# Kernel optimization log

Measured on AMD Instinct MI355X. Metric: run time of the kernel, lower is better.

The kernel has to match this reference:

```python
import jax, jax.numpy as jnp
import numpy as np

N_CHILDS = 50000
N_EDGES = 500000
NODE_FEAT = 256
NUM_SEM = 57
HID = 256
EDGE_FEAT = 64
EDGE_TYPES = 4
NUM_ITERS = 2


def setup_inputs() -> dict:
    key = jax.random.key(0)
    ks = jax.random.split(key, 12)
    d_in = NODE_FEAT + NUM_SEM            # 313
    d_ne = 2 * HID + EDGE_FEAT + EDGE_TYPES  # 580
    d_par = HID * (NUM_ITERS + 1)         # 768
    def lin(k, fan_in, fan_out):
        kw, kb = jax.random.split(k)
        s = 1.0 / np.sqrt(fan_in)
        return (jax.random.uniform(kw, (fan_in, fan_out), jnp.float32, -s, s),
                jax.random.uniform(kb, (fan_out,), jnp.float32, -s, s))
    W_child, b_child = lin(ks[0], d_in, HID)
    W_ne0, b_ne0 = lin(ks[1], d_ne, HID)
    W_ne1, b_ne1 = lin(ks[2], d_ne, HID)
    W_parent, b_parent = lin(ks[3], d_par, NODE_FEAT)
    return {
        "child_feats": jax.random.normal(ks[4], (1, N_CHILDS, d_in), jnp.float32),
        "child_exists": jnp.ones((1, N_CHILDS, 1), jnp.float32),
        "edge_type_onehot": jax.random.normal(ks[5], (1, N_EDGES, EDGE_TYPES), jnp.float32),
        "edge_feats": jax.random.normal(ks[6], (1, N_EDGES, EDGE_FEAT), jnp.float32),
        "edge_indices": jax.random.randint(ks[7], (1, N_EDGES, 2), 0, N_CHILDS, jnp.int64),
        "W_child": W_child, "b_child": b_child,
        "W_ne0": W_ne0, "b_ne0": b_ne0,
        "W_ne1": W_ne1, "b_ne1": b_ne1,
        "W_parent": W_parent, "b_parent": b_parent,
    }


def reference(child_feats, child_exists, edge_type_onehot, edge_feats, edge_indices,
              W_child, b_child, W_ne0, b_ne0, W_ne1, b_ne1, W_parent, b_parent):
    n = child_feats.shape[1]
    # node embedding: linear + relu, mask non-existent children
    x = jax.nn.relu(jnp.einsum('bnd,dh->bnh', child_feats, W_child) + b_child)
    x = x * child_exists                              # [1, N, H]
    iter_parent = [x.max(axis=1)]                     # symmetric_type == 'max'
    ef = jnp.concatenate([edge_type_onehot, edge_feats], axis=2)[0]  # [E, 4+64]
    src = edge_indices[0, :, 0]
    dst = edge_indices[0, :, 1]
    cnt = jax.ops.segment_sum(jnp.ones((src.shape[0],), x.dtype), src, num_segments=n)
    denom = jnp.maximum(cnt, 1.0)[:, None]            # scatter_mean clamp
    for W, b in ((W_ne0, b_ne0), (W_ne1, b_ne1)):
        nef = jnp.concatenate([x[0, src], x[0, dst], ef], axis=1)  # [E, 580]
        nef = jax.nn.relu(nef @ W + b)                # [E, H]
        # edge_symmetric_type == 'avg': scatter_mean over source index
        x = (jax.ops.segment_sum(nef, src, num_segments=n) / denom)[None]
        iter_parent.append(x.max(axis=1))
    parent = jnp.concatenate(iter_parent, axis=1)     # [1, H*(iters+1)]
    return jax.nn.relu(parent @ W_parent + b_parent)  # [1, node_feat_size]
```

## Files before the change

kernel.cpp:

```cpp
#include <hip/hip_runtime.h>

#define NC   50000
#define NE   500000
#define NEP  (NE + 64)
#define DIN  313
#define DNE  580
#define KPC  320
#define KB   96
#define NB_SCAN 196

typedef __attribute__((ext_vector_type(8))) short bf16x8;
typedef __attribute__((ext_vector_type(4))) float f32x4;

static __device__ __forceinline__ unsigned short f2bf(float f) {
    unsigned u = __float_as_uint(f);
    unsigned r = (u + 0x7fff + ((u >> 16) & 1)) >> 16;
    return (unsigned short)r;
}
static __device__ __forceinline__ float bf2f(unsigned short u) {
    return __uint_as_float(((unsigned)u) << 16);
}
static __device__ __forceinline__ void gload_lds16(const unsigned short* g, unsigned short* l) {
    __builtin_amdgcn_global_load_lds(
        (const __attribute__((address_space(1))) unsigned int*)(g),
        (__attribute__((address_space(3))) unsigned int*)(l), 16, 0, 0);
}

__global__ __launch_bounds__(256) void prep_w_kernel(
    const float* __restrict__ W0, const float* __restrict__ W1,
    const float* __restrict__ Wc,
    unsigned short* __restrict__ Wpt, unsigned short* __restrict__ Wbt,
    unsigned short* __restrict__ Wct)
{
    int b = blockIdx.x;
    if (b < 1024) {
        int layer = b >> 9, n2 = b & 511;
        const float* W = layer ? W1 : W0;
        unsigned short* dst = Wpt + (size_t)layer * 512 * 256 + (size_t)n2 * 256;
        int t = threadIdx.x;
        int ch = t >> 5, s = (t >> 3) & 3, j = t & 7;
        int gk = ch * 32 + ((s ^ (n2 & 3)) * 8) + j;
        float v = (n2 < 256) ? W[(size_t)gk * 256 + n2] : W[(size_t)(256 + gk) * 256 + (n2 - 256)];
        dst[t] = f2bf(v);
    } else if (b < 1536) {
        int idx = b - 1024;
        int layer = idx >> 8, n = idx & 255;
        const float* W = layer ? W1 : W0;
        unsigned short* dst = Wbt + (size_t)layer * 256 * KB + (size_t)n * KB;
        int t = threadIdx.x;
        if (t < KB) {
            int ch = t >> 5, s = (t >> 3) & 3, j = t & 7;
            int gk = ch * 32 + ((s ^ (n & 3)) * 8) + j;
            float v = (512 + gk < DNE) ? W[(size_t)(512 + gk) * 256 + n] : 0.0f;
            dst[t] = f2bf(v);
        }
    } else {
        int n = b - 1536;
        unsigned short* dst = Wct + (size_t)n * KPC;
        for (int t = threadIdx.x; t < KPC; t += 256) {
            int ch = t >> 5, s = (t >> 3) & 3, j = t & 7;
            int gk = ch * 32 + ((s ^ (n & 3)) * 8) + j;
            float v = (gk < DIN) ? Wc[(size_t)gk * 256 + n] : 0.0f;
            dst[t] = f2bf(v);
        }
    }
}

__global__ __launch_bounds__(256, 4) void child_mfma_kernel(
    const float* __restrict__ cf, const float* __restrict__ exists,
    const unsigned short* __restrict__ Wct, const float* __restrict__ bias,
    unsigned short* __restrict__ xb, float* __restrict__ pmax)
{
    __shared__ unsigned short sA[64][40];
    __shared__ unsigned short sB[256][32];
    __shared__ float smax[256];

    const int tid = threadIdx.x, lane = tid & 63, wid = tid >> 6;
    const int wm = wid >> 1, wn = wid & 1, l15 = lane & 15, l4 = lane >> 4;
    const int node0 = blockIdx.x * 64;
    const int arow = tid >> 2, s3 = tid & 3;

    smax[tid] = 0.0f;

    f32x4 acc[2][8];
    #pragma unroll
    for (int mi = 0; mi < 2; ++mi)
        #pragma unroll
        for (int ni = 0; ni < 8; ++ni)
            acc[mi][ni] = (f32x4){0.f, 0.f, 0.f, 0.f};

    int nodeA = node0 + arow; if (nodeA >= NC) nodeA = NC - 1;

    for (int ch = 0; ch < 10; ++ch) {
        #pragma unroll
        for (int i = 0; i < 4; ++i) {
            int n = (wid << 6) + (i << 4) + (lane >> 2);
            gload_lds16(Wct + (size_t)n * KPC + ch * 32 + (lane & 3) * 8,
                        &sB[(wid << 6) + (i << 4)][0]);
        }
        {
            int gk0 = ch * 32 + s3 * 8;
            union { unsigned short u[8]; int4 v; } pk;
            #pragma unroll
            for (int j = 0; j < 8; ++j) {
                int gk = gk0 + j;
                float f = (gk < DIN) ? cf[(size_t)nodeA * DIN + gk] : 0.0f;
                pk.u[j] = f2bf(f);
            }
            *(int4*)&sA[arow][s3 * 8] = pk.v;
        }
        __syncthreads();
        bf16x8 af[2];
        #pragma unroll
        for (int mi = 0; mi < 2; ++mi)
            af[mi] = *(const bf16x8*)&sA[wm * 32 + mi * 16 + l15][l4 * 8];
        #pragma unroll
        for (int ni = 0; ni < 8; ++ni) {
            int n = wn * 128 + ni * 16 + l15;
            bf16x8 bfr = *(const bf16x8*)&sB[n][(l4 ^ (n & 3)) * 8];
            acc[0][ni] = __builtin_amdgcn_mfma_f32_16x16x32_bf16(af[0], bfr, acc[0][ni], 0, 0, 0);
            acc[1][ni] = __builtin_amdgcn_mfma_f32_16x16x32_bf16(af[1], bfr, acc[1][ni], 0, 0, 0);
        }
        __syncthreads();
    }

    float bv[8];
    #pragma unroll
    for (int ni = 0; ni < 8; ++ni) bv[ni] = bias[wn * 128 + ni * 16 + l15];
    float cmax[8];
    #pragma unroll
    for (int ni = 0; ni < 8; ++ni) cmax[ni] = 0.0f;

    #pragma unroll
    for (int mi = 0; mi < 2; ++mi) {
        #pragma unroll
        for (int r = 0; r < 4; ++r) {
            int node = node0 + wm * 32 + mi * 16 + l4 * 4 + r;
            if (node < NC) {
                float ex = exists[node];
                #pragma unroll
                for (int ni = 0; ni < 8; ++ni) {
                    float v = fmaxf(acc[mi][ni][r] + bv[ni], 0.f) * ex;
                    xb[(size_t)node * 256 + wn * 128 + ni * 16 + l15] = f2bf(v);
                    cmax[ni] = fmaxf(cmax[ni], v);
                }
            }
        }
    }
    #pragma unroll
    for (int ni = 0; ni < 8; ++ni)
        atomicMax((unsigned int*)&smax[wn * 128 + ni * 16 + l15], __float_as_uint(cmax[ni]));
    __syncthreads();
    atomicMax((unsigned int*)&pmax[tid], __float_as_uint(smax[tid]));
}

__global__ __launch_bounds__(256, 3) void node_gemm_kernel(
    const unsigned short* __restrict__ xb,
    const unsigned short* __restrict__ Wpt,
    unsigned short* __restrict__ yp)
{
    __shared__ unsigned short sA[2][64][40];
    __shared__ unsigned short sB[2][256][32];

    const int tid = threadIdx.x, lane = tid & 63, wid = tid >> 6;
    const int wm = wid >> 1, wn = wid & 1, l15 = lane & 15, l4 = lane >> 4;
    const int node0 = blockIdx.x * 64;
    const int n0 = blockIdx.y * 256;
    const int arow = tid >> 2, s3 = tid & 3;

    int nodeA = node0 + arow; if (nodeA >= NC) nodeA = NC - 1;

    f32x4 acc[2][8];
    #pragma unroll
    for (int mi = 0; mi < 2; ++mi)
        #pragma unroll
        for (int ni = 0; ni < 8; ++ni)
            acc[mi][ni] = (f32x4){0.f, 0.f, 0.f, 0.f};

    #pragma unroll
    for (int i = 0; i < 4; ++i) {
        int n = (wid << 6) + (i << 4) + (lane >> 2);
        gload_lds16(Wpt + (size_t)(n0 + n) * 256 + (lane & 3) * 8, &sB[0][(wid << 6) + (i << 4)][0]);
    }
    *(int4*)&sA[0][arow][s3 * 8] = *(const int4*)(xb + (size_t)nodeA * 256 + s3 * 8);
    __syncthreads();

    int buf = 0;
    for (int ch = 0; ch < 8; ++ch) {
        const int nch = ch + 1;
        int4 areg;
        if (nch < 8) {
            #pragma unroll
            for (int i = 0; i < 4; ++i) {
                int n = (wid << 6) + (i << 4) + (lane >> 2);
                gload_lds16(Wpt + (size_t)(n0 + n) * 256 + nch * 32 + (lane & 3) * 8,
                            &sB[buf ^ 1][(wid << 6) + (i << 4)][0]);
            }
            areg = *(const int4*)(xb + (size_t)nodeA * 256 + nch * 32 + s3 * 8);
        }
        bf16x8 af[2];
        #pragma unroll
        for (int mi = 0; mi < 2; ++mi)
            af[mi] = *(const bf16x8*)&sA[buf][wm * 32 + mi * 16 + l15][l4 * 8];
        #pragma unroll
        for (int ni = 0; ni < 8; ++ni) {
            int n = wn * 128 + ni * 16 + l15;
            bf16x8 bfr = *(const bf16x8*)&sB[buf][n][(l4 ^ (n & 3)) * 8];
            acc[0][ni] = __builtin_amdgcn_mfma_f32_16x16x32_bf16(af[0], bfr, acc[0][ni], 0, 0, 0);
            acc[1][ni] = __builtin_amdgcn_mfma_f32_16x16x32_bf16(af[1], bfr, acc[1][ni], 0, 0, 0);
        }
        if (nch < 8) *(int4*)&sA[buf ^ 1][arow][s3 * 8] = areg;
        __syncthreads();
        buf ^= 1;
    }

    #pragma unroll
    for (int mi = 0; mi < 2; ++mi) {
        #pragma unroll
        for (int r = 0; r < 4; ++r) {
            int node = node0 + wm * 32 + mi * 16 + l4 * 4 + r;
            if (node < NC) {
                #pragma unroll
                for (int ni = 0; ni < 8; ++ni)
                    yp[(size_t)node * 512 + n0 + wn * 128 + ni * 16 + l15] = f2bf(acc[mi][ni][r]);
            }
        }
    }
}

__global__ __launch_bounds__(256, 3) void node_gemm_scaled_kernel(
    const float* __restrict__ accb, const float* __restrict__ invv,
    const unsigned short* __restrict__ Wpt,
    unsigned short* __restrict__ yp)
{
    __shared__ unsigned short sA[2][64][40];
    __shared__ unsigned short sB[2][256][32];

    const int tid = threadIdx.x, lane = tid & 63, wid = tid >> 6;
    const int wm = wid >> 1, wn = wid & 1, l15 = lane & 15, l4 = lane >> 4;
    const int node0 = blockIdx.x * 64;
    const int n0 = blockIdx.y * 256;
    const int arow = tid >> 2, s3 = tid & 3;

    int nodeA = node0 + arow; if (nodeA >= NC) nodeA = NC - 1;
    const float inv_n = invv[nodeA];

    f32x4 acc[2][8];
    #pragma unroll
    for (int mi = 0; mi < 2; ++mi)
        #pragma unroll
        for (int ni = 0; ni < 8; ++ni)
            acc[mi][ni] = (f32x4){0.f, 0.f, 0.f, 0.f};

    #pragma unroll
    for (int i = 0; i < 4; ++i) {
        int n = (wid << 6) + (i << 4) + (lane >> 2);
        gload_lds16(Wpt + (size_t)(n0 + n) * 256 + (lane & 3) * 8, &sB[0][(wid << 6) + (i << 4)][0]);
    }
    {
        float4 a0 = *(const float4*)(accb + (size_t)nodeA * 256 + s3 * 8);
        float4 a1 = *(const float4*)(accb + (size_t)nodeA * 256 + s3 * 8 + 4);
        union { unsigned short u[8]; int4 v; } pk;
        pk.u[0]=f2bf(a0.x*inv_n); pk.u[1]=f2bf(a0.y*inv_n); pk.u[2]=f2bf(a0.z*inv_n); pk.u[3]=f2bf(a0.w*inv_n);
        pk.u[4]=f2bf(a1.x*inv_n); pk.u[5]=f2bf(a1.y*inv_n); pk.u[6]=f2bf(a1.z*inv_n); pk.u[7]=f2bf(a1.w*inv_n);
        *(int4*)&sA[0][arow][s3 * 8] = pk.v;
    }
    __syncthreads();

    int buf = 0;
    for (int ch = 0; ch < 8; ++ch) {
        const int nch = ch + 1;
        float4 f4a, f4b;
        if (nch < 8) {
            #pragma unroll
            for (int i = 0; i < 4; ++i) {
                int n = (wid << 6) + (i << 4) + (lane >> 2);
                gload_lds16(Wpt + (size_t)(n0 + n) * 256 + nch * 32 + (lane & 3) * 8,
                            &sB[buf ^ 1][(wid << 6) + (i << 4)][0]);
            }
            f4a = *(const float4*)(accb + (size_t)nodeA * 256 + nch * 32 + s3 * 8);
            f4b = *(const float4*)(accb + (size_t)nodeA * 256 + nch * 32 + s3 * 8 + 4);
        }
        bf16x8 af[2];
        #pragma unroll
        for (int mi = 0; mi < 2; ++mi)
            af[mi] = *(const bf16x8*)&sA[buf][wm * 32 + mi * 16 + l15][l4 * 8];
        #pragma unroll
        for (int ni = 0; ni < 8; ++ni) {
            int n = wn * 128 + ni * 16 + l15;
            bf16x8 bfr = *(const bf16x8*)&sB[buf][n][(l4 ^ (n & 3)) * 8];
            acc[0][ni] = __builtin_amdgcn_mfma_f32_16x16x32_bf16(af[0], bfr, acc[0][ni], 0, 0, 0);
            acc[1][ni] = __builtin_amdgcn_mfma_f32_16x16x32_bf16(af[1], bfr, acc[1][ni], 0, 0, 0);
        }
        if (nch < 8) {
            union { unsigned short u[8]; int4 v; } pk;
            pk.u[0]=f2bf(f4a.x*inv_n); pk.u[1]=f2bf(f4a.y*inv_n); pk.u[2]=f2bf(f4a.z*inv_n); pk.u[3]=f2bf(f4a.w*inv_n);
            pk.u[4]=f2bf(f4b.x*inv_n); pk.u[5]=f2bf(f4b.y*inv_n); pk.u[6]=f2bf(f4b.z*inv_n); pk.u[7]=f2bf(f4b.w*inv_n);
            *(int4*)&sA[buf ^ 1][arow][s3 * 8] = pk.v;
        }
        __syncthreads();
        buf ^= 1;
    }

    #pragma unroll
    for (int mi = 0; mi < 2; ++mi) {
        #pragma unroll
        for (int r = 0; r < 4; ++r) {
            int node = node0 + wm * 32 + mi * 16 + l4 * 4 + r;
            if (node < NC) {
                #pragma unroll
                for (int ni = 0; ni < 8; ++ni)
                    yp[(size_t)node * 512 + n0 + wn * 128 + ni * 16 + l15] = f2bf(acc[mi][ni][r]);
            }
        }
    }
}

__global__ __launch_bounds__(256) void count_int_kernel(
    const int* __restrict__ eidx, int* __restrict__ icnt)
{
    int t = blockIdx.x * 256 + threadIdx.x;
    if (t < NE) atomicAdd(&icnt[eidx[2 * t]], 1);
}

__global__ __launch_bounds__(256) void scan1_kernel(
    const int* __restrict__ icnt, int* __restrict__ part)
{
    __shared__ int sd[256];
    int i = blockIdx.x * 256 + threadIdx.x;
    sd[threadIdx.x] = (i < NC) ? icnt[i] : 0;
    __syncthreads();
    for (int d = 128; d > 0; d >>= 1) {
        if (threadIdx.x < d) sd[threadIdx.x] += sd[threadIdx.x + d];
        __syncthreads();
    }
    if (threadIdx.x == 0) part[blockIdx.x] = sd[0];
}

__global__ void scan2_kernel(int* __restrict__ part)
{
    if (threadIdx.x == 0) {
        int acc = 0;
        for (int i = 0; i < NB_SCAN; ++i) { int v = part[i]; part[i] = acc; acc += v; }
    }
}

__global__ __launch_bounds__(256) void scan3_kernel(
    const int* __restrict__ icnt, const int* __restrict__ part,
    int* __restrict__ cur)
{
    __shared__ int sc[256];
    const int t = threadIdx.x;
    int i = blockIdx.x * 256 + t;
    int val = (i < NC) ? icnt[i] : 0;
    sc[t] = val;
    __syncthreads();
    for (int d = 1; d < 256; d <<= 1) {
        int x = (t >= d) ? sc[t - d] : 0;
        __syncthreads();
        sc[t] += x;
        __syncthreads();
    }
    if (i < NC) cur[i] = part[blockIdx.x] + sc[t] - val;
}

__global__ __launch_bounds__(256) void bin_kernel(
    const int* __restrict__ eidx, int* __restrict__ cur, int* __restrict__ perm)
{
    int t = blockIdx.x * 256 + threadIdx.x;
    if (t < NE) {
        int s = eidx[2 * t];
        int p = atomicAdd(&cur[s], 1);
        perm[p] = t;
    }
}

__global__ __launch_bounds__(256) void inv_kernel(
    const int* __restrict__ icnt, float* __restrict__ inv)
{
    int t = blockIdx.x * 256 + threadIdx.x;
    if (t < NC) inv[t] = 1.0f / fmaxf((float)icnt[t], 1.0f);
}

__global__ __launch_bounds__(256) void ef_prep_kernel(
    const float* __restrict__ eto, const float* __restrict__ efe,
    const int* __restrict__ perm, const int* __restrict__ eidx,
    unsigned short* __restrict__ efc01, unsigned short* __restrict__ efc2,
    int* __restrict__ esrc, int* __restrict__ edst)
{
    int p = blockIdx.x * 256 + threadIdx.x;
    if (p >= NE) return;
    int e = perm[p];
    esrc[p] = eidx[2 * e];
    edst[p] = eidx[2 * e + 1];
    const float* efr = efe + (size_t)e * 64;

    union { unsigned short u[8]; int4 v; } pk;
    {
        float4 a = *(const float4*)(eto + (size_t)e * 4);
        float4 b = *(const float4*)(efr + 0);
        pk.u[0]=f2bf(a.x); pk.u[1]=f2bf(a.y); pk.u[2]=f2bf(a.z); pk.u[3]=f2bf(a.w);
        pk.u[4]=f2bf(b.x); pk.u[5]=f2bf(b.y); pk.u[6]=f2bf(b.z); pk.u[7]=f2bf(b.w);
        *(int4*)(efc01 + (size_t)p * 32) = pk.v;
    }
    #pragma unroll
    for (int g = 1; g < 4; ++g) {
        float4 a = *(const float4*)(efr + g * 8 - 4);
        float4 b = *(const float4*)(efr + g * 8);
        pk.u[0]=f2bf(a.x); pk.u[1]=f2bf(a.y); pk.u[2]=f2bf(a.z); pk.u[3]=f2bf(a.w);
        pk.u[4]=f2bf(b.x); pk.u[5]=f2bf(b.y); pk.u[6]=f2bf(b.z); pk.u[7]=f2bf(b.w);
        *(int4*)(efc01 + (size_t)p * 32 + g * 8) = pk.v;
    }
    #pragma unroll
    for (int g = 0; g < 4; ++g) {
        float4 a = *(const float4*)(efr + 28 + g * 8);
        float4 b = *(const float4*)(efr + 32 + g * 8);
        pk.u[0]=f2bf(a.x); pk.u[1]=f2bf(a.y); pk.u[2]=f2bf(a.z); pk.u[3]=f2bf(a.w);
        pk.u[4]=f2bf(b.x); pk.u[5]=f2bf(b.y); pk.u[6]=f2bf(b.z); pk.u[7]=f2bf(b.w);
        *(int4*)(efc01 + ((size_t)NEP + p) * 32 + g * 8) = pk.v;
    }
    {
        float4 a = *(const float4*)(efr + 60);
        pk.u[0]=f2bf(a.x); pk.u[1]=f2bf(a.y); pk.u[2]=f2bf(a.z); pk.u[3]=f2bf(a.w);
        pk.u[4]=0; pk.u[5]=0; pk.u[6]=0; pk.u[7]=0;
        *(int4*)(efc2 + (size_t)p * 8) = pk.v;
    }
}

#define LOAD16(B, YT, YM)                                              \
    _Pragma("unroll")                                                  \
    for (int r = 0; r < 16; ++r) {                                     \
        int row = (B) * 16 + r;                                        \
        int sr_ = s_src[row];                                          \
        if (sr_ != ldsrc) {                   \
            ytPrev = bf2f(yp[((unsigned)sr_ << 9) + (unsigned)col]);   \
            ldsrc = sr_;                                               \
        }                                                              \
        YT[r] = ytPrev;                                                \
        YM[r] = bf2f(yp[((unsigned)s_dst[row] << 9) + 256u + (unsigned)col]); \
    }

#define WALK16(B, YT, YM)                                              \
    _Pragma("unroll")                                                  \
    for (int r = 0; r < 16; ++r) {                                     \
        int row = (B) * 16 + r;                                        \
        float v = 0.0f;                                                \
        if (e0 + row < NE)                                             \
            v = fmaxf(bf2f(epb[row][col]) + YT[r] + YM[r] + b_col, 0.f); \
        int sr = s_src[row];                                           \
        if (sr != curn) {                                              \
            if (rstart > 0) accb[(size_t)curn * 256 + col] = run;      \
            else            atomicAdd(&accb[(size_t)curn * 256 + col], run); \
            curn = sr; run = v; rstart = row;                          \
        } else {                                                       \
            run += v;                                                  \
        }                                                              \
    }

__global__ __launch_bounds__(256, 4) void combine_efc_kernel(
    const unsigned short* __restrict__ yp,
    const unsigned short* __restrict__ efc01,
    const unsigned short* __restrict__ efc2,
    const int* __restrict__ esrc, const int* __restrict__ edst,
    const unsigned short* __restrict__ Wbt,
    const float* __restrict__ bias,
    float* __restrict__ accb)
{
    __shared__ __align__(16) unsigned char smem[34816];
    unsigned short (*sA01)[64][32] = (unsigned short (*)[64][32])(smem);
    unsigned short (*sA2)[8]       = (unsigned short (*)[8])(smem + 8192);
    unsigned short (*sW)[32]       = (unsigned short (*)[32])(smem + 9216);
    unsigned short (*epb)[272]     = (unsigned short (*)[272])(smem);
    __shared__ int s_src[64], s_dst[64];

    const int tid = threadIdx.x;
    const int nwg = gridDim.x;
    const int q = nwg >> 3, rr = nwg & 7;
    const int xcd = blockIdx.x & 7, within = blockIdx.x >> 3;
    const int bid = (xcd < rr ? xcd * (q + 1) : rr * (q + 1) + (xcd - rr) * q) + within;
    const int e0 = bid * 64;

    const int lane = tid & 63;
    const int wid  = tid >> 6;
    const int wm   = wid >> 1;
    const int wn   = wid & 1;
    const int l15  = lane & 15;
    const int l4   = lane >> 4;

    if (tid < 64) {
        int e = e0 + tid; if (e > NE - 1) e = NE - 1;
        s_src[tid] = esrc[e];
        s_dst[tid] = edst[e];
    }
    gload_lds16(efc01 + ((size_t)e0 + wid * 16) * 32 + lane * 8, &sA01[0][wid * 16][0]);
    gload_lds16(efc01 + ((size_t)NEP + e0 + wid * 16) * 32 + lane * 8, &sA01[1][wid * 16][0]);
    if (wid == 0)
        gload_lds16(efc2 + (size_t)e0 * 8 + lane * 8, &sA2[0][0]);
    #pragma unroll
    for (int i = 0; i < 4; ++i) {
        gload_lds16(Wbt + (size_t)((wid << 6) + (i << 4) + (lane >> 2)) * KB + (lane & 3) * 8,
                    &sW[(wid << 6) + (i << 4)][0]);
    }
    __syncthreads();

    f32x4 acc[2][8];
    #pragma unroll
    for (int mi = 0; mi < 2; ++mi)
        #pragma unroll
        for (int ni = 0; ni < 8; ++ni)
            acc[mi][ni] = (f32x4){0.f, 0.f, 0.f, 0.f};

    #pragma unroll
    for (int ch = 0; ch < 3; ++ch) {
        if (ch > 0) {
            __syncthreads();
            #pragma unroll
            for (int i = 0; i < 4; ++i) {
                gload_lds16(Wbt + (size_t)((wid << 6) + (i << 4) + (lane >> 2)) * KB + ch * 32 + (lane & 3) * 8,
                            &sW[(wid << 6) + (i << 4)][0]);
            }
            __syncthreads();
        }
        bf16x8 af0, af1;
        if (ch < 2) {
            af0 = *(const bf16x8*)&sA01[ch][wm * 32 + l15][l4 * 8];
            af1 = *(const bf16x8*)&sA01[ch][wm * 32 + 16 + l15][l4 * 8];
        } else {
            bf16x8 z = (bf16x8){0,0,0,0,0,0,0,0};
            bf16x8 a0 = *(const bf16x8*)&sA2[wm * 32 + l15][0];
            bf16x8 a1 = *(const bf16x8*)&sA2[wm * 32 + 16 + l15][0];
            af0 = (l4 == 0) ? a0 : z;
            af1 = (l4 == 0) ? a1 : z;
        }
        #pragma unroll
        for (int ni = 0; ni < 8; ++ni) {
            int n = wn * 128 + ni * 16 + l15;
            bf16x8 bfr = *(const bf16x8*)&sW[n][(l4 ^ (n & 3)) * 8];
            acc[0][ni] = __builtin_amdgcn_mfma_f32_16x16x32_bf16(af0, bfr, acc[0][ni], 0, 0, 0);
            acc[1][ni] = __builtin_amdgcn_mfma_f32_16x16x32_bf16(af1, bfr, acc[1][ni], 0, 0, 0);
        }
    }
    __syncthreads();

    #pragma unroll
    for (int mi = 0; mi < 2; ++mi)
        #pragma unroll
        for (int ni = 0; ni < 8; ++ni)
            #pragma unroll
            for (int r = 0; r < 4; ++r)
                epb[wm * 32 + mi * 16 + l4 * 4 + r][wn * 128 + ni * 16 + l15] = f2bf(acc[mi][ni][r]);

    const int col = tid;
    const float b_col = bias[col];
    int ldsrc = -1;
    float ytPrev = 0.f;
    float ytA[16], ymA[16], ytB[16], ymB[16];
    LOAD16(0, ytA, ymA)
    LOAD16(1, ytB, ymB)
    __syncthreads();

    int curn = s_src[0];
    int rstart = 0;
    float run = 0.f;

    WALK16(0, ytA, ymA)
    LOAD16(2, ytA, ymA)
    WALK16(1, ytB, ymB)
    LOAD16(3, ytB, ymB)
    WALK16(2, ytA, ymA)
    WALK16(3, ytB, ymB)

    atomicAdd(&accb[(size_t)curn * 256 + col], run);
}

__global__ __launch_bounds__(256, 3) void combine_f32_kernel(
    const unsigned short* __restrict__ yp,
    const float* __restrict__ eto, const float* __restrict__ efe,
    const int* __restrict__ eidx, const int* __restrict__ perm,
    const unsigned short* __restrict__ Wbt,
    const float* __restrict__ bias,
    float* __restrict__ accb)
{
    __shared__ unsigned short sA[3][64][40];
    __shared__ unsigned short sW[2][256][32];
    __shared__ int s_src[64], s_dst[64], s_perm[64];

    const int tid = threadIdx.x;
    const int nwg = gridDim.x;
    const int q = nwg >> 3, rr = nwg & 7;
    const int xcd = blockIdx.x & 7, within = blockIdx.x >> 3;
    const int bid = (xcd < rr ? xcd * (q + 1) : rr * (q + 1) + (xcd - rr) * q) + within;
    const int e0 = bid * 64;

    if (tid < 64) {
        int ee = e0 + tid; if (ee >= NE) ee = NE - 1;
        int e = perm[ee];
        s_perm[tid] = e;
        s_src[tid] = eidx[2 * e];
        s_dst[tid] = eidx[2 * e + 1];
    }
    const int lane = tid & 63;
    const int wid  = tid >> 6;
    const int wm   = wid >> 1;
    const int wn   = wid & 1;
    const int l15  = lane & 15;
    const int l4   = lane >> 4;
    const int arow = tid >> 2;
    const int s3   = tid & 3;

    f32x4 acc[2][8];
    #pragma unroll
    for (int mi = 0; mi < 2; ++mi)
        #pragma unroll
        for (int ni = 0; ni < 8; ++ni)
            acc[mi][ni] = (f32x4){0.f, 0.f, 0.f, 0.f};

    #pragma unroll
    for (int i = 0; i < 4; ++i) {
        int n = (wid << 6) + (i << 4) + (lane >> 2);
        gload_lds16(Wbt + (size_t)n * KB + (lane & 3) * 8, &sW[0][(wid << 6) + (i << 4)][0]);
    }
    __syncthreads();

    const int my_e = s_perm[arow];
    #pragma unroll
    for (int ch = 0; ch < 3; ++ch) {
        int g0 = ch * 32 + s3 * 8;
        union { unsigned short u[8]; int4 v; } pk;
        #pragma unroll
        for (int j = 0; j < 8; ++j) {
            int g = g0 + j;
            float f = 0.0f;
            if (g < 4)       f = eto[(size_t)my_e * 4 + g];
            else if (g < 68) f = efe[(size_t)my_e * 64 + (g - 4)];
            pk.u[j] = f2bf(f);
        }
        *(int4*)&sA[ch][arow][s3 * 8] = pk.v;
    }
    __syncthreads();

    int buf = 0;
    #pragma unroll
    for (int ch = 0; ch < 3; ++ch) {
        if (ch + 1 < 3) {
            #pragma unroll
            for (int i = 0; i < 4; ++i) {
                int n = (wid << 6) + (i << 4) + (lane >> 2);
                gload_lds16(Wbt + (size_t)n * KB + (ch + 1) * 32 + (lane & 3) * 8,
                            &sW[buf ^ 1][(wid << 6) + (i << 4)][0]);
            }
        }
        bf16x8 af[2];
        #pragma unroll
        for (int mi = 0; mi < 2; ++mi)
            af[mi] = *(const bf16x8*)&sA[ch][wm * 32 + mi * 16 + l15][l4 * 8];
        #pragma unroll
        for (int ni = 0; ni < 8; ++ni) {
            int n = wn * 128 + ni * 16 + l15;
            bf16x8 bfr = *(const bf16x8*)&sW[buf][n][(l4 ^ (n & 3)) * 8];
            acc[0][ni] = __builtin_amdgcn_mfma_f32_16x16x32_bf16(af[0], bfr, acc[0][ni], 0, 0, 0);
            acc[1][ni] = __builtin_amdgcn_mfma_f32_16x16x32_bf16(af[1], bfr, acc[1][ni], 0, 0, 0);
        }
        __syncthreads();
        buf ^= 1;
    }

    float (*ep)[258] = (float (*)[258])(&sW[0][0][0]);
    const int col = tid;
    const float b_col = bias[col];

    int curn = s_src[0];
    int rstart = 0;
    float run = 0.f;
    #pragma unroll
    for (int c = 0; c < 4; ++c) {
        if (wm == (c >> 1)) {
            const int mi = c & 1;
            #pragma unroll
            for (int ni = 0; ni < 8; ++ni) {
                #pragma unroll
                for (int r = 0; r < 4; ++r)
                    ep[l4 * 4 + r][wn * 128 + ni * 16 + l15] = acc[mi][ni][r];
            }
        }
        float yt[16], ym[16];
        #pragma unroll
        for (int r = 0; r < 16; ++r) {
            int row = c * 16 + r;
            yt[r] = bf2f(yp[(size_t)s_src[row] * 512 + col]);
            ym[r] = bf2f(yp[(size_t)s_dst[row] * 512 + 256 + col]);
        }
        __syncthreads();
        #pragma unroll
        for (int r = 0; r < 16; ++r) {
            int row = c * 16 + r;
            float v = 0.0f;
            if (e0 + row < NE)
                v = fmaxf(ep[r][col] + yt[r] + ym[r] + b_col, 0.f);
            int sr = s_src[row];
            if (sr != curn) {
                if (rstart > 0) accb[(size_t)curn * 256 + col] = run;
                else            atomicAdd(&accb[(size_t)curn * 256 + col], run);
                curn = sr; run = v; rstart = row;
            } else {
                run += v;
            }
        }
        __syncthreads();
    }
    atomicAdd(&accb[(size_t)curn * 256 + col], run);
}

__global__ __launch_bounds__(256) void finalize_kernel(
    const float* __restrict__ src, const float* __restrict__ inv,
    unsigned short* __restrict__ xb_out, float* __restrict__ pmax, int n)
{
    const int tid = threadIdx.x;
    int i0 = blockIdx.x * 128;
    int iend = i0 + 128; if (iend > n) iend = n;
    float m = 0.0f;
    for (int i = i0; i < iend; ++i) {
        float v = src[(size_t)i * 256 + tid];
        v *= inv[i];
        xb_out[(size_t)i * 256 + tid] = f2bf(v);
        m = fmaxf(m, v);
    }
    atomicMax((unsigned int*)&pmax[tid], __float_as_uint(m));
}

__global__ __launch_bounds__(256) void pmax_only_kernel(
    const float* __restrict__ src, const float* __restrict__ inv,
    float* __restrict__ pmax, int n)
{
    const int tid = threadIdx.x;
    int i0 = blockIdx.x * 128;
    int iend = i0 + 128; if (iend > n) iend = n;
    float m = 0.0f;
    for (int i = i0; i < iend; ++i)
        m = fmaxf(m, src[(size_t)i * 256 + tid] * inv[i]);
    atomicMax((unsigned int*)&pmax[tid], __float_as_uint(m));
}

__global__ __launch_bounds__(256) void parent_kernel(
    const float* __restrict__ pmax, const float* __restrict__ W,
    const float* __restrict__ bias, float* __restrict__ out)
{
    __shared__ float sp[768];
    const int tid = threadIdx.x;
    for (int i = tid; i < 768; i += 256) sp[i] = pmax[i];
    __syncthreads();
    float s = bias[tid];
    for (int k = 0; k < 768; ++k) s = fmaf(sp[k], W[(size_t)k * 256 + tid], s);
    out[tid] = fmaxf(s, 0.f);
}

extern "C" void kernel_launch(void* const* d_in, const int* in_sizes, int n_in,
                              void* d_out, int out_size, void* d_ws, size_t ws_size,
                              hipStream_t stream)
{
    const float* cf   = (const float*)d_in[0];
    const float* ex   = (const float*)d_in[1];
    const float* eto  = (const float*)d_in[2];
    const float* efe  = (const float*)d_in[3];
    const int*   eidx = (const int*)d_in[4];
    const float* Wc   = (const float*)d_in[5];
    const float* bc   = (const float*)d_in[6];
    const float* W0   = (const float*)d_in[7];
    const float* b0   = (const float*)d_in[8];
    const float* W1   = (const float*)d_in[9];
    const float* b1   = (const float*)d_in[10];
    const float* Wp   = (const float*)d_in[11];
    const float* bp   = (const float*)d_in[12];

    float*          accb = (float*)d_ws;
    float*          invv = accb + (size_t)NC * 256;
    float*          pmax = invv + NC;
    unsigned short* xb   = (unsigned short*)(pmax + 768);
    unsigned short* yp   = xb + (size_t)NC * 256;
    unsigned short* Wpt  = yp + (size_t)NC * 512;
    unsigned short* Wbt  = Wpt + (size_t)2 * 512 * 256;
    unsigned short* Wct  = Wbt + (size_t)2 * 256 * KB;
    int*            icnt = (int*)(Wct + (size_t)256 * KPC);
    int*            part = icnt + NC;
    int*            curb = part + 256;
    int*            perm = curb + NC;
    unsigned short* efc01 = (unsigned short*)(perm + NE);
    unsigned short* efc2  = efc01 + (size_t)2 * NEP * 32;
    int*            esrc  = (int*)(efc2 + (size_t)NEP * 8);
    int*            edst  = esrc + NE;
    size_t need = (size_t)((char*)(edst + NE) - (char*)d_ws);
    const bool use_efc = (ws_size >= need);

    hipMemsetAsync(pmax, 0, 768 * sizeof(float), stream);
    hipMemsetAsync(icnt, 0, NC * sizeof(int), stream);

    prep_w_kernel<<<1792, 256, 0, stream>>>(W0, W1, Wc, Wpt, Wbt, Wct);
    child_mfma_kernel<<<(NC + 63) / 64, 256, 0, stream>>>(cf, ex, Wct, bc, xb, pmax);

    count_int_kernel<<<(NE + 255) / 256, 256, 0, stream>>>(eidx, icnt);
    scan1_kernel<<<NB_SCAN, 256, 0, stream>>>(icnt, part);
    scan2_kernel<<<1, 64, 0, stream>>>(part);
    scan3_kernel<<<NB_SCAN, 256, 0, stream>>>(icnt, part, curb);
    bin_kernel<<<(NE + 255) / 256, 256, 0, stream>>>(eidx, curb, perm);
    inv_kernel<<<(NC + 255) / 256, 256, 0, stream>>>(icnt, invv);
    if (use_efc)
        ef_prep_kernel<<<(NE + 255) / 256, 256, 0, stream>>>(eto, efe, perm, eidx, efc01, efc2, esrc, edst);

    const int nwg = (NE + 63) / 64;
    if (use_efc) {
        node_gemm_kernel<<<dim3((NC + 63) / 64, 2), 256, 0, stream>>>(xb, Wpt, yp);
        hipMemsetAsync(accb, 0, (size_t)NC * 256 * sizeof(float), stream);
        combine_efc_kernel<<<nwg, 256, 0, stream>>>(
            yp, efc01, efc2, esrc, edst, Wbt, b0, accb);
        pmax_only_kernel<<<(NC + 127) / 128, 256, 0, stream>>>(accb, invv, pmax + 256, NC);
        node_gemm_scaled_kernel<<<dim3((NC + 63) / 64, 2), 256, 0, stream>>>(
            accb, invv, Wpt + (size_t)512 * 256, yp);
        hipMemsetAsync(accb, 0, (size_t)NC * 256 * sizeof(float), stream);
        combine_efc_kernel<<<nwg, 256, 0, stream>>>(
            yp, efc01, efc2, esrc, edst, Wbt + (size_t)256 * KB, b1, accb);
        pmax_only_kernel<<<(NC + 127) / 128, 256, 0, stream>>>(accb, invv, pmax + 512, NC);
    } else {
        for (int it = 0; it < 2; ++it) {
            node_gemm_kernel<<<dim3((NC + 63) / 64, 2), 256, 0, stream>>>(
                xb, Wpt + (size_t)it * 512 * 256, yp);
            hipMemsetAsync(accb, 0, (size_t)NC * 256 * sizeof(float), stream);
            combine_f32_kernel<<<nwg, 256, 0, stream>>>(
                yp, eto, efe, eidx, perm,
                Wbt + (size_t)it * 256 * KB, it ? b1 : b0, accb);
            finalize_kernel<<<(NC + 127) / 128, 256, 0, stream>>>(accb, invv, xb, pmax + 256 * (it + 1), NC);
        }
    }
    parent_kernel<<<1, 256, 0, stream>>>(pmax, Wp, bp, (float*)d_out);
}
```

Baseline: 658.2 us.

## Fuse first-iteration parent max into scaled node GEMM; drop src-load dedup

Computes the per-feature max of the scaled aggregate inside node_gemm_scaled_kernel. It uses LDS atomicMax on float bits, then one global atomicMax per column, so the separate pmax_only_kernel launch and its extra full read of accb are removed. It also simplifies the combine kernel's LOAD16 to load the source row every time instead of reusing the previous value when consecutive src indices repeat. This trades redundant gathers for fewer branches. The uint-compare max is only valid for non-negative values. That holds here because the aggregates come from ReLU outputs, and smax starts at zero. Every column of the block is covered, but each blockIdx.y computes the same max redundantly.

```diff
diff --git a/kernel.cpp b/kernel.cpp
--- a/kernel.cpp
+++ b/kernel.cpp
@@ -231,10 +231,11 @@
 __global__ __launch_bounds__(256, 3) void node_gemm_scaled_kernel(
     const float* __restrict__ accb, const float* __restrict__ invv,
     const unsigned short* __restrict__ Wpt,
-    unsigned short* __restrict__ yp)
+    unsigned short* __restrict__ yp, float* __restrict__ pmax0)
 {
     __shared__ unsigned short sA[2][64][40];
     __shared__ unsigned short sB[2][256][32];
+    __shared__ float smax[256];
 
     const int tid = threadIdx.x, lane = tid & 63, wid = tid >> 6;
     const int wm = wid >> 1, wn = wid & 1, l15 = lane & 15, l4 = lane >> 4;
@@ -242,6 +243,8 @@
     const int n0 = blockIdx.y * 256;
     const int arow = tid >> 2, s3 = tid & 3;
 
+    smax[tid] = 0.0f;
+
     int nodeA = node0 + arow; if (nodeA >= NC) nodeA = NC - 1;
     const float inv_n = invv[nodeA];
 
@@ -260,10 +263,21 @@
     {
         float4 a0 = *(const float4*)(accb + (size_t)nodeA * 256 + s3 * 8);
         float4 a1 = *(const float4*)(accb + (size_t)nodeA * 256 + s3 * 8 + 4);
+        float v0=a0.x*inv_n, v1=a0.y*inv_n, v2=a0.z*inv_n, v3=a0.w*inv_n;
+        float v4=a1.x*inv_n, v5=a1.y*inv_n, v6=a1.z*inv_n, v7=a1.w*inv_n;
         union { unsigned short u[8]; int4 v; } pk;
-        pk.u[0]=f2bf(a0.x*inv_n); pk.u[1]=f2bf(a0.y*inv_n); pk.u[2]=f2bf(a0.z*inv_n); pk.u[3]=f2bf(a0.w*inv_n);
-        pk.u[4]=f2bf(a1.x*inv_n); pk.u[5]=f2bf(a1.y*inv_n); pk.u[6]=f2bf(a1.z*inv_n); pk.u[7]=f2bf(a1.w*inv_n);
+        pk.u[0]=f2bf(v0); pk.u[1]=f2bf(v1); pk.u[2]=f2bf(v2); pk.u[3]=f2bf(v3);
+        pk.u[4]=f2bf(v4); pk.u[5]=f2bf(v5); pk.u[6]=f2bf(v6); pk.u[7]=f2bf(v7);
         *(int4*)&sA[0][arow][s3 * 8] = pk.v;
+        int c0 = s3 * 8;
+        atomicMax((unsigned int*)&smax[c0+0], __float_as_uint(v0));
+        atomicMax((unsigned int*)&smax[c0+1], __float_as_uint(v1));
+        atomicMax((unsigned int*)&smax[c0+2], __float_as_uint(v2));
+        atomicMax((unsigned int*)&smax[c0+3], __float_as_uint(v3));
+        atomicMax((unsigned int*)&smax[c0+4], __float_as_uint(v4));
+        atomicMax((unsigned int*)&smax[c0+5], __float_as_uint(v5));
+        atomicMax((unsigned int*)&smax[c0+6], __float_as_uint(v6));
+        atomicMax((unsigned int*)&smax[c0+7], __float_as_uint(v7));
     }
     __syncthreads();
 
@@ -293,10 +307,21 @@
             acc[1][ni] = __builtin_amdgcn_mfma_f32_16x16x32_bf16(af[1], bfr, acc[1][ni], 0, 0, 0);
         }
         if (nch < 8) {
+            float v0=f4a.x*inv_n, v1=f4a.y*inv_n, v2=f4a.z*inv_n, v3=f4a.w*inv_n;
+            float v4=f4b.x*inv_n, v5=f4b.y*inv_n, v6=f4b.z*inv_n, v7=f4b.w*inv_n;
             union { unsigned short u[8]; int4 v; } pk;
-            pk.u[0]=f2bf(f4a.x*inv_n); pk.u[1]=f2bf(f4a.y*inv_n); pk.u[2]=f2bf(f4a.z*inv_n); pk.u[3]=f2bf(f4a.w*inv_n);
-            pk.u[4]=f2bf(f4b.x*inv_n); pk.u[5]=f2bf(f4b.y*inv_n); pk.u[6]=f2bf(f4b.z*inv_n); pk.u[7]=f2bf(f4b.w*inv_n);
+            pk.u[0]=f2bf(v0); pk.u[1]=f2bf(v1); pk.u[2]=f2bf(v2); pk.u[3]=f2bf(v3);
+            pk.u[4]=f2bf(v4); pk.u[5]=f2bf(v5); pk.u[6]=f2bf(v6); pk.u[7]=f2bf(v7);
             *(int4*)&sA[buf ^ 1][arow][s3 * 8] = pk.v;
+            int c0 = nch * 32 + s3 * 8;
+            atomicMax((unsigned int*)&smax[c0+0], __float_as_uint(v0));
+            atomicMax((unsigned int*)&smax[c0+1], __float_as_uint(v1));
+            atomicMax((unsigned int*)&smax[c0+2], __float_as_uint(v2));
+            atomicMax((unsigned int*)&smax[c0+3], __float_as_uint(v3));
+            atomicMax((unsigned int*)&smax[c0+4], __float_as_uint(v4));
+            atomicMax((unsigned int*)&smax[c0+5], __float_as_uint(v5));
+            atomicMax((unsigned int*)&smax[c0+6], __float_as_uint(v6));
+            atomicMax((unsigned int*)&smax[c0+7], __float_as_uint(v7));
         }
         __syncthreads();
         buf ^= 1;
@@ -314,6 +339,7 @@
             }
         }
     }
+    atomicMax((unsigned int*)&pmax0[tid], __float_as_uint(smax[tid]));
 }
 
 __global__ __launch_bounds__(256) void count_int_kernel(
@@ -431,12 +457,7 @@
     _Pragma("unroll")                                                  \
     for (int r = 0; r < 16; ++r) {                                     \
         int row = (B) * 16 + r;                                        \
-        int sr_ = s_src[row];                                          \
-        if (sr_ != ldsrc) {                   \
-            ytPrev = bf2f(yp[((unsigned)sr_ << 9) + (unsigned)col]);   \
-            ldsrc = sr_;                                               \
-        }                                                              \
-        YT[r] = ytPrev;                                                \
+        YT[r] = bf2f(yp[((unsigned)s_src[row] << 9) + (unsigned)col]); \
         YM[r] = bf2f(yp[((unsigned)s_dst[row] << 9) + 256u + (unsigned)col]); \
     }
 
@@ -552,8 +573,6 @@
 
     const int col = tid;
     const float b_col = bias[col];
-    int ldsrc = -1;
-    float ytPrev = 0.f;
     float ytA[16], ymA[16], ytB[16], ymB[16];
     LOAD16(0, ytA, ymA)
     LOAD16(1, ytB, ymB)
@@ -812,9 +831,8 @@
         hipMemsetAsync(accb, 0, (size_t)NC * 256 * sizeof(float), stream);
         combine_efc_kernel<<<nwg, 256, 0, stream>>>(
             yp, efc01, efc2, esrc, edst, Wbt, b0, accb);
-        pmax_only_kernel<<<(NC + 127) / 128, 256, 0, stream>>>(accb, invv, pmax + 256, NC);
         node_gemm_scaled_kernel<<<dim3((NC + 63) / 64, 2), 256, 0, stream>>>(
-            accb, invv, Wpt + (size_t)512 * 256, yp);
+            accb, invv, Wpt + (size_t)512 * 256, yp, pmax + 256);
         hipMemsetAsync(accb, 0, (size_t)NC * 256 * sizeof(float), stream);
         combine_efc_kernel<<<nwg, 256, 0, stream>>>(
             yp, efc01, efc2, esrc, edst, Wbt + (size_t)256 * KB, b1, accb);
```

Result: faster. 604.1 us, median of 3 (-8.2%).
